# Kernel tuning notes

Measured on AMD Instinct MI355X. Metric: run time of the kernel, lower is better.

The kernel has to match this reference:

```python
import jax, jax.numpy as jnp
import numpy as np

N_NODES = 100000
N_EDGES = 1600000
NODE_DIM = 128
HIDDEN = 128
OUT_DIM = 128
N_GRAPHS = 64
LN_EPS = 1e-5


def setup_inputs() -> dict:
    key = jax.random.key(0)
    ks = jax.random.split(key, 14)

    def lin(k, fan_in, fan_out):
        bound = 1.0 / np.sqrt(fan_in)
        kw, kb = jax.random.split(k)
        W = jax.random.uniform(kw, (fan_in, fan_out), jnp.float32, -bound, bound)
        b = jax.random.uniform(kb, (fan_out,), jnp.float32, -bound, bound)
        return W, b

    node_features = jax.random.normal(ks[0], (N_NODES, NODE_DIM), jnp.float32)
    edge_index = jax.random.randint(ks[1], (2, N_EDGES), 0, N_NODES, jnp.int32)
    batch = jnp.sort(jax.random.randint(ks[2], (N_NODES,), 0, N_GRAPHS, jnp.int32))

    W1, b1 = lin(ks[3], NODE_DIM, HIDDEN)
    W2, b2 = lin(ks[4], HIDDEN, HIDDEN)
    W3, b3 = lin(ks[5], HIDDEN, OUT_DIM)
    Wm1, bm1 = lin(ks[6], OUT_DIM, HIDDEN)
    Wm2, bm2 = lin(ks[7], HIDDEN, OUT_DIM)
    ln_g = jnp.ones((OUT_DIM,), jnp.float32)
    ln_b = jnp.zeros((OUT_DIM,), jnp.float32)

    return dict(node_features=node_features, edge_index=edge_index, batch=batch,
                W1=W1, b1=b1, W2=W2, b2=b2, W3=W3, b3=b3,
                Wm1=Wm1, bm1=bm1, Wm2=Wm2, bm2=bm2, ln_g=ln_g, ln_b=ln_b)


def _gcn_precompute(edge_index, n_nodes):
    # Add self-loops; symmetric degree normalization (PyG GCNConv semantics).
    loops = jnp.arange(n_nodes, dtype=edge_index.dtype)
    src = jnp.concatenate([edge_index[0], loops])
    dst = jnp.concatenate([edge_index[1], loops])
    deg = jax.ops.segment_sum(jnp.ones_like(dst, jnp.float32), dst, num_segments=n_nodes)
    dinv = jax.lax.rsqrt(deg)  # deg >= 1 thanks to self-loops
    norm = dinv[src] * dinv[dst]  # [E + N]
    return src, dst, norm


def _gcn_layer(x, W, b, src, dst, norm, n_nodes):
    xw = x @ W                              # [N, F_out]
    msg = norm[:, None] * xw[src]           # [E+N, F_out] gather
    agg = jax.ops.segment_sum(msg, dst, num_segments=n_nodes)  # scatter-add
    return agg + b


def reference(node_features, edge_index, batch,
              W1, b1, W2, b2, W3, b3, Wm1, bm1, Wm2, bm2, ln_g, ln_b):
    n_nodes = node_features.shape[0]
    src, dst, norm = _gcn_precompute(edge_index, n_nodes)

    x = jax.nn.relu(_gcn_layer(node_features, W1, b1, src, dst, norm, n_nodes))
    x = jax.nn.relu(_gcn_layer(x, W2, b2, src, dst, norm, n_nodes))
    x = _gcn_layer(x, W3, b3, src, dst, norm, n_nodes)  # no relu on last layer

    # global mean pool per graph
    sums = jax.ops.segment_sum(x, batch, num_segments=N_GRAPHS)
    cnts = jax.ops.segment_sum(jnp.ones((n_nodes,), x.dtype), batch, num_segments=N_GRAPHS)
    g = sums / jnp.maximum(cnts, 1.0)[:, None]  # [G, OUT_DIM]

    # global reasoner MLP + LayerNorm
    h = jax.nn.relu(g @ Wm1 + bm1)
    y = h @ Wm2 + bm2
    mu = jnp.mean(y, axis=-1, keepdims=True)
    var = jnp.var(y, axis=-1, keepdims=True)
    y = (y - mu) * jax.lax.rsqrt(var + LN_EPS) * ln_g + ln_b
    return y
```

## Files before the change

### kernel.cpp

```cpp
#include <hip/hip_runtime.h>

#define FDIM 128
#define LN_EPS 1e-5f
#define NBKT_SHIFT 10
#define BKT_NODES 1024
#define MAXBKT 128
#define CAP_SHIFT 15
#define BKT_CAP 32768

typedef short bf16x8 __attribute__((ext_vector_type(8)));
typedef float f32x4 __attribute__((ext_vector_type(4)));
typedef float f32x2 __attribute__((ext_vector_type(2)));
typedef ushort u16x8 __attribute__((ext_vector_type(8)));
typedef unsigned long long u64;

static __device__ __forceinline__ ushort f2bf(float f) {
    union { float f; unsigned u; } v; v.f = f;
    unsigned r = v.u + 0x7FFFu + ((v.u >> 16) & 1u);
    return (ushort)(r >> 16);
}
static __device__ __forceinline__ float bf2f(ushort h) {
    union { unsigned u; float f; } v; v.u = ((unsigned)h) << 16;
    return v.f;
}
static __device__ __forceinline__ unsigned char f2fp8(float f) {
    return (unsigned char)__builtin_amdgcn_cvt_pk_fp8_f32(f, f, 0u, false);
}
static __device__ __forceinline__ void fp8x8_add(uint2 w, f32x2* acc) {
    acc[0] += __builtin_amdgcn_cvt_pk_f32_fp8(w.x, false);
    acc[1] += __builtin_amdgcn_cvt_pk_f32_fp8(w.x, true);
    acc[2] += __builtin_amdgcn_cvt_pk_f32_fp8(w.y, false);
    acc[3] += __builtin_amdgcn_cvt_pk_f32_fp8(w.y, true);
}


__launch_bounds__(256)
__global__ void k_bkt_scatter(const int* __restrict__ src, const int* __restrict__ dst,
                              int* __restrict__ bcur, unsigned* __restrict__ bktA,
                              int E, int nbkt) {
    __shared__ int h[2][MAXBKT], lbase[2][MAXBKT], lcur[2][MAXBKT];
    const int t = threadIdx.x;
    const int half = t >> 7;
    for (int i = t; i < 2 * MAXBKT; i += 256) ((int*)h)[i] = 0;
    __syncthreads();
    const int E4 = E >> 2;
    const int4* s4p = (const int4*)src;
    const int4* d4p = (const int4*)dst;
    int4 sv[4], dv[4]; bool ok[4];
#pragma unroll
    for (int r = 0; r < 4; r++) {
        int i4 = blockIdx.x * 1024 + r * 256 + t;
        ok[r] = (i4 < E4);
        if (ok[r]) {
            sv[r] = s4p[i4]; dv[r] = d4p[i4];
            atomicAdd(&h[half][dv[r].x >> NBKT_SHIFT], 1);
            atomicAdd(&h[half][dv[r].y >> NBKT_SHIFT], 1);
            atomicAdd(&h[half][dv[r].z >> NBKT_SHIFT], 1);
            atomicAdd(&h[half][dv[r].w >> NBKT_SHIFT], 1);
        }
    }
    __syncthreads();
    for (int i = t; i < 2 * nbkt; i += 256) {
        const int hh = (i >= nbkt) ? 1 : 0;
        const int b = hh ? (i - nbkt) : i;
        const int c = h[hh][b];
        lbase[hh][b] = c ? ((b << CAP_SHIFT) + atomicAdd(&bcur[b], c)) : 0;
        lcur[hh][b] = 0;
    }
    __syncthreads();
#pragma unroll
    for (int r = 0; r < 4; r++) {
        if (!ok[r]) continue;
        int ss[4] = {sv[r].x, sv[r].y, sv[r].z, sv[r].w};
        int dd[4] = {dv[r].x, dv[r].y, dv[r].z, dv[r].w};
#pragma unroll
        for (int j = 0; j < 4; j++) {
            int b = dd[j] >> NBKT_SHIFT;
            int p = atomicAdd(&lcur[half][b], 1);
            bktA[(size_t)lbase[half][b] + p] =
                ((unsigned)ss[j] << NBKT_SHIFT) | (unsigned)(dd[j] & (BKT_NODES - 1));
        }
    }
}


__launch_bounds__(1024)
__global__ void k_build(const unsigned* __restrict__ bktA, const int* __restrict__ bcur,
                        int2* __restrict__ rowinfo, float* __restrict__ dinv,
                        int* __restrict__ csr_src, int N) {
    __shared__ int cnt[BKT_NODES];
    __shared__ int cur[BKT_NODES];
    __shared__ int wpart[16], wbase[16];
    const int t = threadIdx.x;
    const int b = blockIdx.x;
    const int nb = b << NBKT_SHIFT;
    cnt[t] = 0;
    __syncthreads();
    const int beg = b << CAP_SHIFT;
    const int end = beg + bcur[b];
    for (int i = beg + t; i < end; i += 1024)
        atomicAdd(&cnt[bktA[i] & (BKT_NODES - 1)], 1);
    __syncthreads();
    const int lane = t & 63, wv = t >> 6;
    const int my = cnt[t];
    int x = my;
#pragma unroll
    for (int off = 1; off < 64; off <<= 1) {
        int y = __shfl_up(x, off, 64);
        if (lane >= off) x += y;
    }
    if (lane == 63) wpart[wv] = x;
    __syncthreads();
    if (t == 0) {
        int s = 0;
        for (int w = 0; w < 16; w++) { int tmp = wpart[w]; wbase[w] = s; s += tmp; }
    }
    __syncthreads();
    const int incl = x + wbase[wv];
    const int rbeg = beg + incl - my;
    cur[t] = rbeg;
    const int n = nb + t;
    if (n < N) {
        rowinfo[n] = make_int2(rbeg, my);
        dinv[n] = rsqrtf((float)(my + 1));
    }
    __syncthreads();
    for (int i = beg + t; i < end; i += 1024) {
        unsigned pr = bktA[i];
        int d = pr & (BKT_NODES - 1);
        int p = atomicAdd(&cur[d], 1);
        csr_src[p] = (int)(pr >> NBKT_SHIFT);
    }
}


__global__ void k_prep_w(const float* __restrict__ Wa, const float* __restrict__ Wb,
                         const float* __restrict__ Wc, ushort* __restrict__ Wt) {
    int idx = blockIdx.x * 256 + threadIdx.x;
    int layer = idx >> 14;
    int r = idx & 16383;
    int nn = r >> 7, kk = r & 127;
    const float* W = (layer == 0) ? Wa : (layer == 1) ? Wb : Wc;
    Wt[idx] = f2bf(W[kk * 128 + nn]);
}


template<bool F32IN>
__launch_bounds__(256)
__global__ void k_gemm(const void* __restrict__ Xv, const ushort* __restrict__ Wt,
                       const float* __restrict__ dinv, unsigned char* __restrict__ C,
                       int N) {
    __shared__ __align__(16) ushort As[128][136];
    __shared__ ushort Ws[128][136];
    const int t = threadIdx.x;
    const int row0 = blockIdx.x * 128;

#pragma unroll
    for (int i = 0; i < 8; i++) {
        int c = t + i * 256;
        int r = c >> 4, c8 = (c & 15) * 8;
        *(bf16x8*)&Ws[r][c8] = *(const bf16x8*)&Wt[r * 128 + c8];
    }
    if (F32IN) {
        const float* X = (const float*)Xv;
#pragma unroll
        for (int i = 0; i < 8; i++) {
            int c = t + i * 256;
            int r = c >> 4, c8 = (c & 15) * 8;
            int row = row0 + r;
            bf16x8 pk = {0, 0, 0, 0, 0, 0, 0, 0};
            if (row < N) {
                const float* sp = X + (size_t)row * FDIM + c8;
                float4 u0 = *(const float4*)(sp);
                float4 u1 = *(const float4*)(sp + 4);
                pk[0] = (short)f2bf(u0.x); pk[1] = (short)f2bf(u0.y);
                pk[2] = (short)f2bf(u0.z); pk[3] = (short)f2bf(u0.w);
                pk[4] = (short)f2bf(u1.x); pk[5] = (short)f2bf(u1.y);
                pk[6] = (short)f2bf(u1.z); pk[7] = (short)f2bf(u1.w);
            }
            *(bf16x8*)&As[r][c8] = pk;
        }
    } else {
        const ushort* X = (const ushort*)Xv;
#pragma unroll
        for (int i = 0; i < 8; i++) {
            int c = t + i * 256;
            int r = c >> 4, c8 = (c & 15) * 8;
            int row = row0 + r;
            bf16x8 pk = {0, 0, 0, 0, 0, 0, 0, 0};
            if (row < N) pk = *(const bf16x8*)&X[(size_t)row * FDIM + c8];
            *(bf16x8*)&As[r][c8] = pk;
        }
    }
    __syncthreads();

    const int w = t >> 6, l = t & 63;
    const int m = l & 15, q = l >> 4;
    const int r0 = w * 32;

    bf16x8 a0[4], a1[4];
#pragma unroll
    for (int ks = 0; ks < 4; ks++) {
        a0[ks] = *(const bf16x8*)&As[r0 + m][ks * 32 + q * 8];
        a1[ks] = *(const bf16x8*)&As[r0 + 16 + m][ks * 32 + q * 8];
    }

    f32x4 acc0[8], acc1[8];
#pragma unroll
    for (int ct = 0; ct < 8; ct++) { acc0[ct] = {0, 0, 0, 0}; acc1[ct] = {0, 0, 0, 0}; }

#pragma unroll
    for (int ct = 0; ct < 8; ct++) {
#pragma unroll
        for (int ks = 0; ks < 4; ks++) {
            bf16x8 b = *(const bf16x8*)&Ws[ct * 16 + m][ks * 32 + q * 8];
            acc0[ct] = __builtin_amdgcn_mfma_f32_16x16x32_bf16(a0[ks], b, acc0[ct], 0, 0, 0);
            acc1[ct] = __builtin_amdgcn_mfma_f32_16x16x32_bf16(a1[ks], b, acc1[ct], 0, 0, 0);
        }
    }

    float dv0[4], dv1[4];
#pragma unroll
    for (int r = 0; r < 4; r++) {
        int row = row0 + r0 + q * 4 + r;
        dv0[r] = (row < N) ? dinv[row] : 0.f;
        dv1[r] = (row + 16 < N) ? dinv[row + 16] : 0.f;
    }

    __syncthreads();
    char* Ab = (char*)&As[0][0];
#pragma unroll
    for (int ct = 0; ct < 8; ct++) {
#pragma unroll
        for (int r = 0; r < 4; r++) {
            int rl = r0 + q * 4 + r;
            Ab[rl * 128 + ct * 16 + m] = (char)f2fp8(acc0[ct][r] * dv0[r]);
            Ab[(rl + 16) * 128 + ct * 16 + m] = (char)f2fp8(acc1[ct][r] * dv1[r]);
        }
    }
    __syncthreads();
    const uint4* As4 = (const uint4*)Ab;
#pragma unroll
    for (int i = 0; i < 4; i++) {
        int c = t + i * 256;
        int row = c >> 3;
        int col = (c & 7) * 16;
        int grow = row0 + row;
        if (grow < N) *(uint4*)&C[(size_t)grow * FDIM + col] = As4[c];
    }
}


__launch_bounds__(256)
__global__ void k_aggregate(const unsigned char* __restrict__ xs8,
                            const int2* __restrict__ rowinfo,
                            const int* __restrict__ csr_src, const float* __restrict__ dinv,
                            const float* __restrict__ bias, ushort* __restrict__ out,
                            int N, int do_relu) {
    const int n = (blockIdx.x << 2) + (threadIdx.x >> 6);
    if (n >= N) return;
    const int l = threadIdx.x & 63;
    const int fl = l & 15;
    const int grp = l >> 4;

    const uint2* xsr = (const uint2*)xs8;

    f32x2 acc[4] = {{0, 0}, {0, 0}, {0, 0}, {0, 0}};
    if (grp == 0) {
        uint2 sv = xsr[(size_t)n * 16 + fl];
        fp8x8_add(sv, acc);
    }

    const int2 ri = rowinfo[n];
    const int beg = ri.x;
    const int deg = ri.y;

    for (int base = 0; base < deg; base += 64) {
        const int m = min(64, deg - base);
        int idx = 0;
        if (l < m) idx = csr_src[beg + base + l];
        for (int jb = 0; jb < m; jb += 16) {
            uint2 vb[4]; bool ok[4];
#pragma unroll
            for (int u = 0; u < 4; u++) {
                int j = jb + u * 4 + grp;
                ok[u] = (j < m);
                if (ok[u]) {
                    int s = __shfl(idx, j, 64);
                    vb[u] = xsr[(size_t)s * 16 + fl];
                }
            }
#pragma unroll
            for (int u = 0; u < 4; u++) if (ok[u]) fp8x8_add(vb[u], acc);
        }
    }

    float a[8] = {acc[0][0], acc[0][1], acc[1][0], acc[1][1],
                  acc[2][0], acc[2][1], acc[3][0], acc[3][1]};
#pragma unroll
    for (int k = 0; k < 8; k++) {
        a[k] += __shfl_xor(a[k], 16, 64);
        a[k] += __shfl_xor(a[k], 32, 64);
    }

    if (grp == 0) {
        const float d = dinv[n];
        const float4 b0 = ((const float4*)bias)[fl * 2];
        const float4 b1 = ((const float4*)bias)[fl * 2 + 1];
        const float bb[8] = {b0.x, b0.y, b0.z, b0.w, b1.x, b1.y, b1.z, b1.w};
        u16x8 o;
#pragma unroll
        for (int k = 0; k < 8; k++) {
            float v = d * a[k] + bb[k];
            if (do_relu) v = fmaxf(v, 0.f);
            o[k] = f2bf(v);
        }
        ((u16x8*)out)[(size_t)n * 16 + fl] = o;
    }
}


#define POOL_NODES 128

__launch_bounds__(128)
__global__ void k_pool(const ushort* __restrict__ x3, const int* __restrict__ batch,
                       float* __restrict__ sums, int N) {
    const int t = threadIdx.x;
    const int n0 = blockIdx.x * POOL_NODES;
    if (n0 >= N) return;
    const int n1 = (n0 + POOL_NODES < N) ? n0 + POOL_NODES : N;

    float acc = 0.f;
    int cur = batch[n0];
    for (int n = n0; n < n1; n++) {
        int g = batch[n];
        if (g != cur) {
            atomicAdd(&sums[cur * FDIM + t], acc);
            acc = 0.f;
            cur = g;
        }
        acc += bf2f(x3[(size_t)n * FDIM + t]);
    }
    atomicAdd(&sums[cur * FDIM + t], acc);
}


__launch_bounds__(128)
__global__ void k_final(const float* __restrict__ sums, const int* __restrict__ batch, int N,
                        const float* __restrict__ Wm1, const float* __restrict__ bm1,
                        const float* __restrict__ Wm2, const float* __restrict__ bm2,
                        const float* __restrict__ ln_g, const float* __restrict__ ln_b,
                        float* __restrict__ out) {
    const int g = blockIdx.x;
    const int t = threadIdx.x;

    int lo = 0, hi = N;
    while (lo < hi) { int mid = (lo + hi) >> 1; if (batch[mid] < g) lo = mid + 1; else hi = mid; }
    int lo2 = lo, hi2 = N;
    while (lo2 < hi2) { int mid = (lo2 + hi2) >> 1; if (batch[mid] < g + 1) lo2 = mid + 1; else hi2 = mid; }
    float cnt = (float)(lo2 - lo);

    float gl = sums[g * FDIM + t] / fmaxf(cnt, 1.0f);

    __shared__ float gbuf[FDIM];
    __shared__ float hbuf[FDIM];
    __shared__ float wsum[4];
    gbuf[t] = gl;
    __syncthreads();

    float h = bm1[t];
#pragma unroll 8
    for (int k = 0; k < FDIM; k++) h += gbuf[k] * Wm1[k * FDIM + t];
    h = fmaxf(h, 0.f);
    hbuf[t] = h;
    __syncthreads();

    float y = bm2[t];
#pragma unroll 8
    for (int k = 0; k < FDIM; k++) y += hbuf[k] * Wm2[k * FDIM + t];

    float s = y, s2 = y * y;
#pragma unroll
    for (int off = 32; off > 0; off >>= 1) {
        s += __shfl_down(s, off, 64);
        s2 += __shfl_down(s2, off, 64);
    }
    if ((t & 63) == 0) { wsum[t >> 6] = s; wsum[2 + (t >> 6)] = s2; }
    __syncthreads();
    float sum = wsum[0] + wsum[1];
    float sumsq = wsum[2] + wsum[3];
    float mu = sum * (1.0f / FDIM);
    float var = sumsq * (1.0f / FDIM) - mu * mu;
    float r = rsqrtf(var + LN_EPS);
    out[g * FDIM + t] = (y - mu) * r * ln_g[t] + ln_b[t];
}


extern "C" void kernel_launch(void* const* d_in, const int* in_sizes, int n_in,
                              void* d_out, int out_size, void* d_ws, size_t ws_size,
                              hipStream_t stream) {
    const float* x_in  = (const float*)d_in[0];
    const int*   eidx  = (const int*)d_in[1];
    const int*   batch = (const int*)d_in[2];
    const float* W1 = (const float*)d_in[3];
    const float* b1 = (const float*)d_in[4];
    const float* W2 = (const float*)d_in[5];
    const float* b2 = (const float*)d_in[6];
    const float* W3 = (const float*)d_in[7];
    const float* b3 = (const float*)d_in[8];
    const float* Wm1 = (const float*)d_in[9];
    const float* bm1 = (const float*)d_in[10];
    const float* Wm2 = (const float*)d_in[11];
    const float* bm2 = (const float*)d_in[12];
    const float* ln_g = (const float*)d_in[13];
    const float* ln_b = (const float*)d_in[14];
    float* out = (float*)d_out;

    const int N = in_sizes[0] / FDIM;
    const int E = in_sizes[1] / 2;
    const int G = out_size / FDIM;

    const int* src = eidx;
    const int* dst = eidx + E;

    const int nbkt = (N + BKT_NODES - 1) >> NBKT_SHIFT;

    char* p = (char*)d_ws;
    unsigned* bktA = (unsigned*)p;    p += (size_t)nbkt * BKT_CAP * 4;
    unsigned char* B0q = (unsigned char*)p; p += (size_t)N * FDIM;
    ushort* B1h = (ushort*)p;         p += (size_t)N * FDIM * 2;
    int* csr_src = (int*)p;           p += (size_t)nbkt * BKT_CAP * 4;
    int2* rowinfo = (int2*)p;         p += (size_t)N * 8;
    float* dinv = (float*)p;          p += (size_t)N * 4;
    ushort* Wt = (ushort*)p;          p += 3 * 16384 * 2;
    float* gsums = (float*)p;         p += (size_t)G * FDIM * 4;
    int* bcur = (int*)p;              p += MAXBKT * 4;

    const int TPB = 256;
    dim3 blk(TPB);
    dim3 gAgg((N + 3) / 4);
    dim3 gTile((N + 127) / 128);
    const int nEb = (E + 4095) / 4096;

    k_prep_w<<<dim3(192), blk, 0, stream>>>(W1, W2, W3, Wt);
    hipMemsetAsync(gsums, 0, (size_t)G * FDIM * 4 + MAXBKT * 4, stream);
    k_bkt_scatter<<<dim3(nEb), blk, 0, stream>>>(src, dst, bcur, bktA, E, nbkt);
    k_build<<<dim3(nbkt), dim3(1024), 0, stream>>>(bktA, bcur, rowinfo, dinv, csr_src, N);

    k_gemm<true><<<gTile, blk, 0, stream>>>(x_in, Wt, dinv, B0q, N);
    k_aggregate<<<gAgg, blk, 0, stream>>>(B0q, rowinfo, csr_src, dinv, b1, B1h, N, 1);

    k_gemm<false><<<gTile, blk, 0, stream>>>(B1h, Wt + 16384, dinv, B0q, N);
    k_aggregate<<<gAgg, blk, 0, stream>>>(B0q, rowinfo, csr_src, dinv, b2, B1h, N, 1);

    k_gemm<false><<<gTile, blk, 0, stream>>>(B1h, Wt + 32768, dinv, B0q, N);
    k_aggregate<<<gAgg, blk, 0, stream>>>(B0q, rowinfo, csr_src, dinv, b3, B1h, N, 0);

    k_pool<<<dim3((N + POOL_NODES - 1) / POOL_NODES), dim3(FDIM), 0, stream>>>(B1h, batch, gsums, N);
    k_final<<<dim3(G), dim3(FDIM), 0, stream>>>(gsums, batch, N, Wm1, bm1, Wm2, bm2,
                                                ln_g, ln_b, out);
}
```

Measured before the change: 437.1 us.

## Store layer activations and weights in FP8, add FP8 MFMA GEMM path

Aggregate outputs are now written as FP8 instead of bf16, and layers 2 and 3 use a new FP8×FP8 MFMA GEMM with FP8-quantized weights, which halves activation traffic between kernels. The aggregation inner loop is restructured into a software-pipelined single-gather loop, and the memset is folded into the weight-prep kernel to remove a launch. The main risk is accuracy loss from quantizing activations and weights to FP8.

```diff
diff --git a/kernel.cpp b/kernel.cpp
--- a/kernel.cpp
+++ b/kernel.cpp
@@ -13,6 +13,7 @@
 typedef float f32x2 __attribute__((ext_vector_type(2)));
 typedef ushort u16x8 __attribute__((ext_vector_type(8)));
 typedef unsigned long long u64;
+typedef long long i64;
 
 static __device__ __forceinline__ ushort f2bf(float f) {
     union { float f; unsigned u; } v; v.f = f;
@@ -25,6 +26,10 @@
 }
 static __device__ __forceinline__ unsigned char f2fp8(float f) {
     return (unsigned char)__builtin_amdgcn_cvt_pk_fp8_f32(f, f, 0u, false);
+}
+static __device__ __forceinline__ float fp8tof(unsigned char b) {
+    f32x2 p = __builtin_amdgcn_cvt_pk_f32_fp8((unsigned)b, false);
+    return p[0];
 }
 static __device__ __forceinline__ void fp8x8_add(uint2 w, f32x2* acc) {
     acc[0] += __builtin_amdgcn_cvt_pk_f32_fp8(w.x, false);
@@ -135,21 +140,28 @@
 
 
 __global__ void k_prep_w(const float* __restrict__ Wa, const float* __restrict__ Wb,
-                         const float* __restrict__ Wc, ushort* __restrict__ Wt) {
+                         const float* __restrict__ Wc, ushort* __restrict__ Wt_b,
+                         unsigned char* __restrict__ Wt8, float* __restrict__ gsums,
+                         int* __restrict__ bcur) {
     int idx = blockIdx.x * 256 + threadIdx.x;
     int layer = idx >> 14;
     int r = idx & 16383;
     int nn = r >> 7, kk = r & 127;
-    const float* W = (layer == 0) ? Wa : (layer == 1) ? Wb : Wc;
-    Wt[idx] = f2bf(W[kk * 128 + nn]);
-}
-
-
-template<bool F32IN>
+    if (layer == 0) {
+        Wt_b[r] = f2bf(Wa[kk * 128 + nn]);
+    } else {
+        const float* W = (layer == 1) ? Wb : Wc;
+        Wt8[(size_t)(layer - 1) * 16384 + r] = f2fp8(W[kk * 128 + nn]);
+    }
+    if (idx < 8192) gsums[idx] = 0.f;
+    if (idx < MAXBKT) bcur[idx] = 0;
+}
+
+
 __launch_bounds__(256)
-__global__ void k_gemm(const void* __restrict__ Xv, const ushort* __restrict__ Wt,
-                       const float* __restrict__ dinv, unsigned char* __restrict__ C,
-                       int N) {
+__global__ void k_gemm_f32(const float* __restrict__ X, const ushort* __restrict__ Wt,
+                           const float* __restrict__ dinv, unsigned char* __restrict__ C,
+                           int N) {
     __shared__ __align__(16) ushort As[128][136];
     __shared__ ushort Ws[128][136];
     const int t = threadIdx.x;
@@ -161,36 +173,22 @@
         int r = c >> 4, c8 = (c & 15) * 8;
         *(bf16x8*)&Ws[r][c8] = *(const bf16x8*)&Wt[r * 128 + c8];
     }
-    if (F32IN) {
-        const float* X = (const float*)Xv;
-#pragma unroll
-        for (int i = 0; i < 8; i++) {
-            int c = t + i * 256;
-            int r = c >> 4, c8 = (c & 15) * 8;
-            int row = row0 + r;
-            bf16x8 pk = {0, 0, 0, 0, 0, 0, 0, 0};
-            if (row < N) {
-                const float* sp = X + (size_t)row * FDIM + c8;
-                float4 u0 = *(const float4*)(sp);
-                float4 u1 = *(const float4*)(sp + 4);
-                pk[0] = (short)f2bf(u0.x); pk[1] = (short)f2bf(u0.y);
-                pk[2] = (short)f2bf(u0.z); pk[3] = (short)f2bf(u0.w);
-                pk[4] = (short)f2bf(u1.x); pk[5] = (short)f2bf(u1.y);
-                pk[6] = (short)f2bf(u1.z); pk[7] = (short)f2bf(u1.w);
-            }
-            *(bf16x8*)&As[r][c8] = pk;
-        }
-    } else {
-        const ushort* X = (const ushort*)Xv;
-#pragma unroll
-        for (int i = 0; i < 8; i++) {
-            int c = t + i * 256;
-            int r = c >> 4, c8 = (c & 15) * 8;
-            int row = row0 + r;
-            bf16x8 pk = {0, 0, 0, 0, 0, 0, 0, 0};
-            if (row < N) pk = *(const bf16x8*)&X[(size_t)row * FDIM + c8];
-            *(bf16x8*)&As[r][c8] = pk;
-        }
+#pragma unroll
+    for (int i = 0; i < 8; i++) {
+        int c = t + i * 256;
+        int r = c >> 4, c8 = (c & 15) * 8;
+        int row = row0 + r;
+        bf16x8 pk = {0, 0, 0, 0, 0, 0, 0, 0};
+        if (row < N) {
+            const float* sp = X + (size_t)row * FDIM + c8;
+            float4 u0 = *(const float4*)(sp);
+            float4 u1 = *(const float4*)(sp + 4);
+            pk[0] = (short)f2bf(u0.x); pk[1] = (short)f2bf(u0.y);
+            pk[2] = (short)f2bf(u0.z); pk[3] = (short)f2bf(u0.w);
+            pk[4] = (short)f2bf(u1.x); pk[5] = (short)f2bf(u1.y);
+            pk[6] = (short)f2bf(u1.z); pk[7] = (short)f2bf(u1.w);
+        }
+        *(bf16x8*)&As[r][c8] = pk;
     }
     __syncthreads();
 
@@ -252,10 +250,89 @@
 
 
 __launch_bounds__(256)
+__global__ void k_gemm_fp8(const unsigned char* __restrict__ X,
+                           const unsigned char* __restrict__ W8,
+                           const float* __restrict__ dinv, unsigned char* __restrict__ C,
+                           int N) {
+    __shared__ __align__(16) unsigned char As[128][144];
+    __shared__ __align__(16) unsigned char Ws[128][144];
+    const int t = threadIdx.x;
+    const int row0 = blockIdx.x * 128;
+
+#pragma unroll
+    for (int i = 0; i < 4; i++) {
+        int c = t + i * 256;
+        int r = c >> 3, col = (c & 7) * 16;
+        *(uint4*)&Ws[r][col] = *(const uint4*)&W8[r * 128 + col];
+        int row = row0 + r;
+        uint4 v = {0, 0, 0, 0};
+        if (row < N) v = *(const uint4*)&X[(size_t)row * FDIM + col];
+        *(uint4*)&As[r][col] = v;
+    }
+    __syncthreads();
+
+    const int w = t >> 6, l = t & 63;
+    const int m = l & 15, q = l >> 4;
+    const int r0 = w * 32;
+
+    i64 a0[4], a1[4];
+#pragma unroll
+    for (int ks = 0; ks < 4; ks++) {
+        a0[ks] = *(const i64*)&As[r0 + m][ks * 32 + q * 8];
+        a1[ks] = *(const i64*)&As[r0 + 16 + m][ks * 32 + q * 8];
+    }
+
+    f32x4 acc0[8], acc1[8];
+#pragma unroll
+    for (int ct = 0; ct < 8; ct++) { acc0[ct] = {0, 0, 0, 0}; acc1[ct] = {0, 0, 0, 0}; }
+
+#pragma unroll
+    for (int ct = 0; ct < 8; ct++) {
+#pragma unroll
+        for (int ks = 0; ks < 4; ks++) {
+            i64 b = *(const i64*)&Ws[ct * 16 + m][ks * 32 + q * 8];
+            acc0[ct] = __builtin_amdgcn_mfma_f32_16x16x32_fp8_fp8(a0[ks], b, acc0[ct], 0, 0, 0);
+            acc1[ct] = __builtin_amdgcn_mfma_f32_16x16x32_fp8_fp8(a1[ks], b, acc1[ct], 0, 0, 0);
+        }
+    }
+
+    float dv0[4], dv1[4];
+#pragma unroll
+    for (int r = 0; r < 4; r++) {
+        int row = row0 + r0 + q * 4 + r;
+        dv0[r] = (row < N) ? dinv[row] : 0.f;
+        dv1[r] = (row + 16 < N) ? dinv[row + 16] : 0.f;
+    }
+
+    __syncthreads();
+    char* Ab = (char*)&As[0][0];
+#pragma unroll
+    for (int ct = 0; ct < 8; ct++) {
+#pragma unroll
+        for (int r = 0; r < 4; r++) {
+            int rl = r0 + q * 4 + r;
+            Ab[rl * 128 + ct * 16 + m] = (char)f2fp8(acc0[ct][r] * dv0[r]);
+            Ab[(rl + 16) * 128 + ct * 16 + m] = (char)f2fp8(acc1[ct][r] * dv1[r]);
+        }
+    }
+    __syncthreads();
+    const uint4* As4 = (const uint4*)Ab;
+#pragma unroll
+    for (int i = 0; i < 4; i++) {
+        int c = t + i * 256;
+        int row = c >> 3;
+        int col = (c & 7) * 16;
+        int grow = row0 + row;
+        if (grow < N) *(uint4*)&C[(size_t)grow * FDIM + col] = As4[c];
+    }
+}
+
+
+__launch_bounds__(256)
 __global__ void k_aggregate(const unsigned char* __restrict__ xs8,
                             const int2* __restrict__ rowinfo,
                             const int* __restrict__ csr_src, const float* __restrict__ dinv,
-                            const float* __restrict__ bias, ushort* __restrict__ out,
+                            const float* __restrict__ bias, unsigned char* __restrict__ out,
                             int N, int do_relu) {
     const int n = (blockIdx.x << 2) + (threadIdx.x >> 6);
     if (n >= N) return;
@@ -279,19 +356,18 @@
         const int m = min(64, deg - base);
         int idx = 0;
         if (l < m) idx = csr_src[beg + base + l];
-        for (int jb = 0; jb < m; jb += 16) {
-            uint2 vb[4]; bool ok[4];
-#pragma unroll
-            for (int u = 0; u < 4; u++) {
-                int j = jb + u * 4 + grp;
-                ok[u] = (j < m);
-                if (ok[u]) {
-                    int s = __shfl(idx, j, 64);
-                    vb[u] = xsr[(size_t)s * 16 + fl];
-                }
+        int j = grp;
+        if (j < m) {
+            int s = __shfl(idx, j, 64);
+            uint2 v = xsr[(size_t)s * 16 + fl];
+#pragma unroll 2
+            for (j += 4; j < m; j += 4) {
+                int s2 = __shfl(idx, j, 64);
+                uint2 v2 = xsr[(size_t)s2 * 16 + fl];
+                fp8x8_add(v, acc);
+                v = v2;
             }
-#pragma unroll
-            for (int u = 0; u < 4; u++) if (ok[u]) fp8x8_add(vb[u], acc);
+            fp8x8_add(v, acc);
         }
     }
 
@@ -308,14 +384,18 @@
         const float4 b0 = ((const float4*)bias)[fl * 2];
         const float4 b1 = ((const float4*)bias)[fl * 2 + 1];
         const float bb[8] = {b0.x, b0.y, b0.z, b0.w, b1.x, b1.y, b1.z, b1.w};
-        u16x8 o;
+        float v[8];
 #pragma unroll
         for (int k = 0; k < 8; k++) {
-            float v = d * a[k] + bb[k];
-            if (do_relu) v = fmaxf(v, 0.f);
-            o[k] = f2bf(v);
-        }
-        ((u16x8*)out)[(size_t)n * 16 + fl] = o;
+            v[k] = d * a[k] + bb[k];
+            if (do_relu) v[k] = fmaxf(v[k], 0.f);
+        }
+        uint2 o;
+        unsigned d0 = __builtin_amdgcn_cvt_pk_fp8_f32(v[0], v[1], 0u, false);
+        o.x = __builtin_amdgcn_cvt_pk_fp8_f32(v[2], v[3], d0, true);
+        unsigned d1 = __builtin_amdgcn_cvt_pk_fp8_f32(v[4], v[5], 0u, false);
+        o.y = __builtin_amdgcn_cvt_pk_fp8_f32(v[6], v[7], d1, true);
+        ((uint2*)out)[(size_t)n * 16 + fl] = o;
     }
 }
 
@@ -323,7 +403,7 @@
 #define POOL_NODES 128
 
 __launch_bounds__(128)
-__global__ void k_pool(const ushort* __restrict__ x3, const int* __restrict__ batch,
+__global__ void k_pool(const unsigned char* __restrict__ x3, const int* __restrict__ batch,
                        float* __restrict__ sums, int N) {
     const int t = threadIdx.x;
     const int n0 = blockIdx.x * POOL_NODES;
@@ -339,7 +419,7 @@
             acc = 0.f;
             cur = g;
         }
-        acc += bf2f(x3[(size_t)n * FDIM + t]);
+        acc += fp8tof(x3[(size_t)n * FDIM + t]);
     }
     atomicAdd(&sums[cur * FDIM + t], acc);
 }
@@ -428,11 +508,12 @@
     char* p = (char*)d_ws;
     unsigned* bktA = (unsigned*)p;    p += (size_t)nbkt * BKT_CAP * 4;
     unsigned char* B0q = (unsigned char*)p; p += (size_t)N * FDIM;
-    ushort* B1h = (ushort*)p;         p += (size_t)N * FDIM * 2;
+    unsigned char* B1q = (unsigned char*)p; p += (size_t)N * FDIM;
     int* csr_src = (int*)p;           p += (size_t)nbkt * BKT_CAP * 4;
     int2* rowinfo = (int2*)p;         p += (size_t)N * 8;
     float* dinv = (float*)p;          p += (size_t)N * 4;
-    ushort* Wt = (ushort*)p;          p += 3 * 16384 * 2;
+    ushort* Wt_b = (ushort*)p;        p += 16384 * 2;
+    unsigned char* Wt8 = (unsigned char*)p; p += 2 * 16384;
     float* gsums = (float*)p;         p += (size_t)G * FDIM * 4;
     int* bcur = (int*)p;              p += MAXBKT * 4;
 
@@ -442,21 +523,20 @@
     dim3 gTile((N + 127) / 128);
     const int nEb = (E + 4095) / 4096;
 
-    k_prep_w<<<dim3(192), blk, 0, stream>>>(W1, W2, W3, Wt);
-    hipMemsetAsync(gsums, 0, (size_t)G * FDIM * 4 + MAXBKT * 4, stream);
+    k_prep_w<<<dim3(192), blk, 0, stream>>>(W1, W2, W3, Wt_b, Wt8, gsums, bcur);
     k_bkt_scatter<<<dim3(nEb), blk, 0, stream>>>(src, dst, bcur, bktA, E, nbkt);
     k_build<<<dim3(nbkt), dim3(1024), 0, stream>>>(bktA, bcur, rowinfo, dinv, csr_src, N);
 
-    k_gemm<true><<<gTile, blk, 0, stream>>>(x_in, Wt, dinv, B0q, N);
-    k_aggregate<<<gAgg, blk, 0, stream>>>(B0q, rowinfo, csr_src, dinv, b1, B1h, N, 1);
-
-    k_gemm<false><<<gTile, blk, 0, stream>>>(B1h, Wt + 16384, dinv, B0q, N);
-    k_aggregate<<<gAgg, blk, 0, stream>>>(B0q, rowinfo, csr_src, dinv, b2, B1h, N, 1);
-
-    k_gemm<false><<<gTile, blk, 0, stream>>>(B1h, Wt + 32768, dinv, B0q, N);
-    k_aggregate<<<gAgg, blk, 0, stream>>>(B0q, rowinfo, csr_src, dinv, b3, B1h, N, 0);
-
-    k_pool<<<dim3((N + POOL_NODES - 1) / POOL_NODES), dim3(FDIM), 0, stream>>>(B1h, batch, gsums, N);
+    k_gemm_f32<<<gTile, blk, 0, stream>>>(x_in, Wt_b, dinv, B0q, N);
+    k_aggregate<<<gAgg, blk, 0, stream>>>(B0q, rowinfo, csr_src, dinv, b1, B1q, N, 1);
+
+    k_gemm_fp8<<<gTile, blk, 0, stream>>>(B1q, Wt8, dinv, B0q, N);
+    k_aggregate<<<gAgg, blk, 0, stream>>>(B0q, rowinfo, csr_src, dinv, b2, B1q, N, 1);
+
+    k_gemm_fp8<<<gTile, blk, 0, stream>>>(B1q, Wt8 + 16384, dinv, B0q, N);
+    k_aggregate<<<gAgg, blk, 0, stream>>>(B0q, rowinfo, csr_src, dinv, b3, B1q, N, 0);
+
+    k_pool<<<dim3((N + POOL_NODES - 1) / POOL_NODES), dim3(FDIM), 0, stream>>>(B1q, batch, gsums, N);
     k_final<<<dim3(G), dim3(FDIM), 0, stream>>>(gsums, batch, N, Wm1, bm1, Wm2, bm2,
                                                 ln_g, ln_b, out);
 }
```

Result: faster. 421.4 us (-3.6%).
